# Optimization experiments

Measured on AMD Instinct MI355X. Metric: run time of the kernel, lower is better.

## Reference

```python
import jax, jax.numpy as jnp
import numpy as np

B, EMB, P, K = 8192, 768, 96, 256
D = EMB // P  # dsub = 8


def setup_inputs() -> dict:
    key = jax.random.key(0)
    k1, k2 = jax.random.split(key)
    vecs = jax.random.normal(k1, (B, EMB), dtype=jnp.float32)
    # torch init: uniform(-1, 1)
    codebook = jax.random.uniform(k2, (P, K, D), dtype=jnp.float32, minval=-1.0, maxval=1.0)
    return {"vecs": vecs, "codebook": codebook}


def reference(vecs, codebook):
    b = vecs.shape[0]
    p, k, d = codebook.shape
    v = vecs.reshape(b, p, d)                                  # [B,P,D]
    # squared distances via expanded quadratic (avoids [B,P,K,D] broadcast):
    # ||v-c||^2 = ||v||^2 - 2 v.c + ||c||^2
    dots = jnp.einsum('bpd,pkd->bpk', v, codebook)             # [B,P,K]
    d2 = (jnp.sum(v * v, axis=-1, keepdims=True)               # [B,P,1]
          - 2.0 * dots
          + jnp.sum(codebook * codebook, axis=-1)[None])       # [1,P,K]
    proba = jax.nn.softmax(-d2, axis=-1)                       # [B,P,K]
    # straight-through hard assignment
    idx = jnp.argmax(proba, axis=-1)                           # [B,P]
    hard = jax.nn.one_hot(idx, k, dtype=proba.dtype)           # [B,P,K]
    ste = jax.lax.stop_gradient(hard - proba) + proba
    # reconstruct from codebook
    out = jnp.einsum('bpk,pkd->bpd', ste, codebook).reshape(b, p * d)
    return out
```

## Files before the change

kernel.cpp:

```cpp
#include <hip/hip_runtime.h>


typedef float f32x2 __attribute__((ext_vector_type(2)));
typedef float f32x4 __attribute__((ext_vector_type(4)));

#define TPB 128
#define KBQ 8

namespace {
constexpr int kB   = 8192;
constexpr int kEMB = 768;
constexpr int kP   = 96;
constexpr int kK   = 256;
constexpr int kD   = 8;
constexpr int kNP  = kK / 2;
constexpr int kNCH = kK / 4;
}

__device__ __forceinline__ f32x2 pk_fma(f32x2 a, f32x2 b, f32x2 c) {
    f32x2 d;
    asm("v_pk_fma_f32 %0, %1, %2, %3" : "=v"(d) : "v"(a), "v"(b), "v"(c));
    return d;
}

__device__ __forceinline__ float c2_of(f32x4 lo, f32x4 hi) {
    float t = lo.x * lo.x;
    t = fmaf(lo.y, lo.y, t);
    t = fmaf(lo.z, lo.z, t);
    t = fmaf(lo.w, lo.w, t);
    t = fmaf(hi.x, hi.x, t);
    t = fmaf(hi.y, hi.y, t);
    t = fmaf(hi.z, hi.z, t);
    t = fmaf(hi.w, hi.w, t);
    return t;
}

__global__ __launch_bounds__(TPB, 2)
void pq_argmin_kernel(const float* __restrict__ vecs,
                      const float* __restrict__ codebook,
                      float* __restrict__ out)
{
    __shared__ alignas(16) f32x4 lds_pairs[kNP][4];
    __shared__ alignas(16) f32x2 lds_c2[kNP];

    const int p = blockIdx.y;
    const int t = threadIdx.x;
    const float* __restrict__ cbp = codebook + (size_t)p * kK * kD;
    const f32x4* cb4 = reinterpret_cast<const f32x4*>(cbp);

    {
        f32x4 a0 = cb4[4 * t + 0];
        f32x4 a1 = cb4[4 * t + 1];
        f32x4 b0 = cb4[4 * t + 2];
        f32x4 b1 = cb4[4 * t + 3];
        lds_pairs[t][0] = f32x4{a0.x, b0.x, a0.y, b0.y};
        lds_pairs[t][1] = f32x4{a0.z, b0.z, a0.w, b0.w};
        lds_pairs[t][2] = f32x4{a1.x, b1.x, a1.y, b1.y};
        lds_pairs[t][3] = f32x4{a1.z, b1.z, a1.w, b1.w};
        lds_c2[t] = f32x2{c2_of(a0, a1), c2_of(b0, b1)};
    }

    const int b0q = blockIdx.x * (TPB * KBQ) + t;
    f32x2 vd[KBQ][kD];
#pragma unroll
    for (int q = 0; q < KBQ; ++q) {
        const f32x4* vp = reinterpret_cast<const f32x4*>(
            vecs + (size_t)(b0q + q * TPB) * kEMB + p * kD);
        f32x4 x = vp[0];
        f32x4 y = vp[1];
        float m0 = -2.0f * x.x, m1 = -2.0f * x.y, m2 = -2.0f * x.z,
              m3 = -2.0f * x.w, m4 = -2.0f * y.x, m5 = -2.0f * y.y,
              m6 = -2.0f * y.z, m7 = -2.0f * y.w;
        vd[q][0] = f32x2{m0, m0}; vd[q][1] = f32x2{m1, m1};
        vd[q][2] = f32x2{m2, m2}; vd[q][3] = f32x2{m3, m3};
        vd[q][4] = f32x2{m4, m4}; vd[q][5] = f32x2{m5, m5};
        vd[q][6] = f32x2{m6, m6}; vd[q][7] = f32x2{m7, m7};
    }
    __syncthreads();

    float best[KBQ];
    int   bch[KBQ];
#pragma unroll
    for (int q = 0; q < KBQ; ++q) {
        best[q] = __builtin_inff();
        bch[q] = 0;
    }

#pragma unroll 2
    for (int ch = 0; ch < kNCH; ++ch) {
        f32x4 p0a = lds_pairs[2 * ch][0];
        f32x4 p0b = lds_pairs[2 * ch][1];
        f32x4 p0c = lds_pairs[2 * ch][2];
        f32x4 p0d = lds_pairs[2 * ch][3];
        f32x4 p1a = lds_pairs[2 * ch + 1][0];
        f32x4 p1b = lds_pairs[2 * ch + 1][1];
        f32x4 p1c = lds_pairs[2 * ch + 1][2];
        f32x4 p1d = lds_pairs[2 * ch + 1][3];
        f32x4 cz = *reinterpret_cast<const f32x4*>(&lds_c2[2 * ch]);

#pragma unroll
        for (int q = 0; q < KBQ; ++q) {
            f32x2 a0 = pk_fma(p0a.xy, vd[q][0], cz.xy);
            a0 = pk_fma(p0a.zw, vd[q][1], a0);
            a0 = pk_fma(p0b.xy, vd[q][2], a0);
            a0 = pk_fma(p0b.zw, vd[q][3], a0);
            a0 = pk_fma(p0c.xy, vd[q][4], a0);
            a0 = pk_fma(p0c.zw, vd[q][5], a0);
            a0 = pk_fma(p0d.xy, vd[q][6], a0);
            a0 = pk_fma(p0d.zw, vd[q][7], a0);

            f32x2 a1 = pk_fma(p1a.xy, vd[q][0], cz.zw);
            a1 = pk_fma(p1a.zw, vd[q][1], a1);
            a1 = pk_fma(p1b.xy, vd[q][2], a1);
            a1 = pk_fma(p1b.zw, vd[q][3], a1);
            a1 = pk_fma(p1c.xy, vd[q][4], a1);
            a1 = pk_fma(p1c.zw, vd[q][5], a1);
            a1 = pk_fma(p1d.xy, vd[q][6], a1);
            a1 = pk_fma(p1d.zw, vd[q][7], a1);

            float m = fminf(fminf(fminf(a0.x, a0.y), a1.x), a1.y);
            if (m < best[q]) {
                best[q] = m;
                bch[q] = ch;
            }
        }
    }

#pragma unroll
    for (int q = 0; q < KBQ; ++q) {
        const int base = bch[q] * 4;
        float s[4];
#pragma unroll
        for (int c = 0; c < 4; ++c) {
            f32x4 lo = cb4[2 * (base + c)];
            f32x4 hi = cb4[2 * (base + c) + 1];
            float cc2 = c2_of(lo, hi);
            float s_ = fmaf(lo.x, vd[q][0].x, cc2);
            s_ = fmaf(lo.y, vd[q][1].x, s_);
            s_ = fmaf(lo.z, vd[q][2].x, s_);
            s_ = fmaf(lo.w, vd[q][3].x, s_);
            s_ = fmaf(hi.x, vd[q][4].x, s_);
            s_ = fmaf(hi.y, vd[q][5].x, s_);
            s_ = fmaf(hi.z, vd[q][6].x, s_);
            s_ = fmaf(hi.w, vd[q][7].x, s_);
            s[c] = s_;
        }
        int idx = base;
        bool fnd = (s[0] == best[q]);
#pragma unroll
        for (int c = 1; c < 4; ++c) {
            bool e = (s[c] == best[q]) && !fnd;
            idx = e ? base + c : idx;
            fnd = fnd || (s[c] == best[q]);
        }
        f32x4 r0 = cb4[2 * idx];
        f32x4 r1 = cb4[2 * idx + 1];
        f32x4* op = reinterpret_cast<f32x4*>(
            out + (size_t)(b0q + q * TPB) * kEMB + p * kD);
        op[0] = r0;
        op[1] = r1;
    }
}

extern "C" void kernel_launch(void* const* d_in, const int* in_sizes, int n_in,
                              void* d_out, int out_size, void* d_ws, size_t ws_size,
                              hipStream_t stream)
{
    const float* vecs     = (const float*)d_in[0];
    const float* codebook = (const float*)d_in[1];
    float* out            = (float*)d_out;

    dim3 grid(kB / (TPB * KBQ), kP, 1);
    dim3 block(TPB, 1, 1);
    hipLaunchKernelGGL(pq_argmin_kernel, grid, block, 0, stream,
                       vecs, codebook, out);
}
```

Baseline: 139.0 us.

## Split codebook search across waves and use op_sel packed FMA broadcasts

Each block now has four waves that share the same 512 vectors, and each wave scans a quarter of the 256 codebook entries. Partial minima are merged through LDS after a second barrier, and each wave then finishes two of the eight vector groups. The query registers are halved by using v_pk_fma_f32 op_sel to broadcast the low or high element instead of keeping duplicated pairs, which lowers register pressure and allows a higher occupancy target. The cost is extra LDS traffic, an additional __syncthreads, and redundant vector loads per wave.

```diff
diff --git a/kernel.cpp b/kernel.cpp
--- a/kernel.cpp
+++ b/kernel.cpp
@@ -4,7 +4,7 @@
 typedef float f32x2 __attribute__((ext_vector_type(2)));
 typedef float f32x4 __attribute__((ext_vector_type(4)));
 
-#define TPB 128
+#define TPB 256
 #define KBQ 8
 
 namespace {
@@ -14,12 +14,19 @@
 constexpr int kK   = 256;
 constexpr int kD   = 8;
 constexpr int kNP  = kK / 2;
-constexpr int kNCH = kK / 4;
-}
-
-__device__ __forceinline__ f32x2 pk_fma(f32x2 a, f32x2 b, f32x2 c) {
+constexpr int kChW = 16;
+}
+
+__device__ __forceinline__ f32x2 pk_bl(f32x2 cp, f32x2 qp, f32x2 acc) {
     f32x2 d;
-    asm("v_pk_fma_f32 %0, %1, %2, %3" : "=v"(d) : "v"(a), "v"(b), "v"(c));
+    asm("v_pk_fma_f32 %0, %1, %2, %3 op_sel:[0,0,0] op_sel_hi:[1,0,1]"
+        : "=v"(d) : "v"(cp), "v"(qp), "v"(acc));
+    return d;
+}
+__device__ __forceinline__ f32x2 pk_bh(f32x2 cp, f32x2 qp, f32x2 acc) {
+    f32x2 d;
+    asm("v_pk_fma_f32 %0, %1, %2, %3 op_sel:[0,1,0] op_sel_hi:[1,1,1]"
+        : "=v"(d) : "v"(cp), "v"(qp), "v"(acc));
     return d;
 }
 
@@ -35,20 +42,25 @@
     return t;
 }
 
-__global__ __launch_bounds__(TPB, 2)
+__global__ __launch_bounds__(TPB, 3)
 void pq_argmin_kernel(const float* __restrict__ vecs,
                       const float* __restrict__ codebook,
                       float* __restrict__ out)
 {
     __shared__ alignas(16) f32x4 lds_pairs[kNP][4];
     __shared__ alignas(16) f32x2 lds_c2[kNP];
-
-    const int p = blockIdx.y;
-    const int t = threadIdx.x;
+    __shared__ float lds_best[4][KBQ][64];
+    __shared__ int   lds_gch [4][KBQ][64];
+
+    const int p    = blockIdx.y;
+    const int t    = threadIdx.x;
+    const int lane = t & 63;
+    const int w    = t >> 6;
+
     const float* __restrict__ cbp = codebook + (size_t)p * kK * kD;
     const f32x4* cb4 = reinterpret_cast<const f32x4*>(cbp);
 
-    {
+    if (t < kNP) {
         f32x4 a0 = cb4[4 * t + 0];
         f32x4 a1 = cb4[4 * t + 1];
         f32x4 b0 = cb4[4 * t + 2];
@@ -60,103 +72,120 @@
         lds_c2[t] = f32x2{c2_of(a0, a1), c2_of(b0, b1)};
     }
 
-    const int b0q = blockIdx.x * (TPB * KBQ) + t;
-    f32x2 vd[KBQ][kD];
+    const int b0q = blockIdx.x * (64 * KBQ) + lane;
+    f32x2 qp[KBQ][4];
 #pragma unroll
     for (int q = 0; q < KBQ; ++q) {
         const f32x4* vp = reinterpret_cast<const f32x4*>(
-            vecs + (size_t)(b0q + q * TPB) * kEMB + p * kD);
+            vecs + (size_t)(b0q + q * 64) * kEMB + p * kD);
         f32x4 x = vp[0];
         f32x4 y = vp[1];
-        float m0 = -2.0f * x.x, m1 = -2.0f * x.y, m2 = -2.0f * x.z,
-              m3 = -2.0f * x.w, m4 = -2.0f * y.x, m5 = -2.0f * y.y,
-              m6 = -2.0f * y.z, m7 = -2.0f * y.w;
-        vd[q][0] = f32x2{m0, m0}; vd[q][1] = f32x2{m1, m1};
-        vd[q][2] = f32x2{m2, m2}; vd[q][3] = f32x2{m3, m3};
-        vd[q][4] = f32x2{m4, m4}; vd[q][5] = f32x2{m5, m5};
-        vd[q][6] = f32x2{m6, m6}; vd[q][7] = f32x2{m7, m7};
+        qp[q][0] = f32x2{-2.0f * x.x, -2.0f * x.y};
+        qp[q][1] = f32x2{-2.0f * x.z, -2.0f * x.w};
+        qp[q][2] = f32x2{-2.0f * y.x, -2.0f * y.y};
+        qp[q][3] = f32x2{-2.0f * y.z, -2.0f * y.w};
     }
     __syncthreads();
 
     float best[KBQ];
-    int   bch[KBQ];
+    int   bgch[KBQ];
 #pragma unroll
     for (int q = 0; q < KBQ; ++q) {
         best[q] = __builtin_inff();
-        bch[q] = 0;
+        bgch[q] = w * kChW;
     }
 
 #pragma unroll 2
-    for (int ch = 0; ch < kNCH; ++ch) {
-        f32x4 p0a = lds_pairs[2 * ch][0];
-        f32x4 p0b = lds_pairs[2 * ch][1];
-        f32x4 p0c = lds_pairs[2 * ch][2];
-        f32x4 p0d = lds_pairs[2 * ch][3];
-        f32x4 p1a = lds_pairs[2 * ch + 1][0];
-        f32x4 p1b = lds_pairs[2 * ch + 1][1];
-        f32x4 p1c = lds_pairs[2 * ch + 1][2];
-        f32x4 p1d = lds_pairs[2 * ch + 1][3];
-        f32x4 cz = *reinterpret_cast<const f32x4*>(&lds_c2[2 * ch]);
+    for (int ch = 0; ch < kChW; ++ch) {
+        const int g  = w * kChW + ch;
+        const int pb = 2 * g;
+        f32x4 P0a = lds_pairs[pb][0];
+        f32x4 P0b = lds_pairs[pb][1];
+        f32x4 P0c = lds_pairs[pb][2];
+        f32x4 P0d = lds_pairs[pb][3];
+        f32x4 P1a = lds_pairs[pb + 1][0];
+        f32x4 P1b = lds_pairs[pb + 1][1];
+        f32x4 P1c = lds_pairs[pb + 1][2];
+        f32x4 P1d = lds_pairs[pb + 1][3];
+        f32x4 cz  = *reinterpret_cast<const f32x4*>(&lds_c2[pb]);
 
 #pragma unroll
         for (int q = 0; q < KBQ; ++q) {
-            f32x2 a0 = pk_fma(p0a.xy, vd[q][0], cz.xy);
-            a0 = pk_fma(p0a.zw, vd[q][1], a0);
-            a0 = pk_fma(p0b.xy, vd[q][2], a0);
-            a0 = pk_fma(p0b.zw, vd[q][3], a0);
-            a0 = pk_fma(p0c.xy, vd[q][4], a0);
-            a0 = pk_fma(p0c.zw, vd[q][5], a0);
-            a0 = pk_fma(p0d.xy, vd[q][6], a0);
-            a0 = pk_fma(p0d.zw, vd[q][7], a0);
-
-            f32x2 a1 = pk_fma(p1a.xy, vd[q][0], cz.zw);
-            a1 = pk_fma(p1a.zw, vd[q][1], a1);
-            a1 = pk_fma(p1b.xy, vd[q][2], a1);
-            a1 = pk_fma(p1b.zw, vd[q][3], a1);
-            a1 = pk_fma(p1c.xy, vd[q][4], a1);
-            a1 = pk_fma(p1c.zw, vd[q][5], a1);
-            a1 = pk_fma(p1d.xy, vd[q][6], a1);
-            a1 = pk_fma(p1d.zw, vd[q][7], a1);
+            f32x2 a0 = pk_bl(P0a.xy, qp[q][0], cz.xy);
+            a0 = pk_bh(P0a.zw, qp[q][0], a0);
+            a0 = pk_bl(P0b.xy, qp[q][1], a0);
+            a0 = pk_bh(P0b.zw, qp[q][1], a0);
+            a0 = pk_bl(P0c.xy, qp[q][2], a0);
+            a0 = pk_bh(P0c.zw, qp[q][2], a0);
+            a0 = pk_bl(P0d.xy, qp[q][3], a0);
+            a0 = pk_bh(P0d.zw, qp[q][3], a0);
+
+            f32x2 a1 = pk_bl(P1a.xy, qp[q][0], cz.zw);
+            a1 = pk_bh(P1a.zw, qp[q][0], a1);
+            a1 = pk_bl(P1b.xy, qp[q][1], a1);
+            a1 = pk_bh(P1b.zw, qp[q][1], a1);
+            a1 = pk_bl(P1c.xy, qp[q][2], a1);
+            a1 = pk_bh(P1c.zw, qp[q][2], a1);
+            a1 = pk_bl(P1d.xy, qp[q][3], a1);
+            a1 = pk_bh(P1d.zw, qp[q][3], a1);
 
             float m = fminf(fminf(fminf(a0.x, a0.y), a1.x), a1.y);
             if (m < best[q]) {
                 best[q] = m;
-                bch[q] = ch;
+                bgch[q] = g;
             }
         }
     }
 
 #pragma unroll
     for (int q = 0; q < KBQ; ++q) {
-        const int base = bch[q] * 4;
+        lds_best[w][q][lane] = best[q];
+        lds_gch [w][q][lane] = bgch[q];
+    }
+    __syncthreads();
+
+#pragma unroll
+    for (int qi = 0; qi < 2; ++qi) {
+        const int q = 2 * w + qi;
+        float bb = lds_best[0][q][lane];
+        int   gc = lds_gch [0][q][lane];
+#pragma unroll
+        for (int wv = 1; wv < 4; ++wv) {
+            float b2 = lds_best[wv][q][lane];
+            int   g2 = lds_gch [wv][q][lane];
+            bool c = (b2 < bb);
+            bb = c ? b2 : bb;
+            gc = c ? g2 : gc;
+        }
+        const int base = gc * 4;
         float s[4];
 #pragma unroll
         for (int c = 0; c < 4; ++c) {
             f32x4 lo = cb4[2 * (base + c)];
             f32x4 hi = cb4[2 * (base + c) + 1];
             float cc2 = c2_of(lo, hi);
-            float s_ = fmaf(lo.x, vd[q][0].x, cc2);
-            s_ = fmaf(lo.y, vd[q][1].x, s_);
-            s_ = fmaf(lo.z, vd[q][2].x, s_);
-            s_ = fmaf(lo.w, vd[q][3].x, s_);
-            s_ = fmaf(hi.x, vd[q][4].x, s_);
-            s_ = fmaf(hi.y, vd[q][5].x, s_);
-            s_ = fmaf(hi.z, vd[q][6].x, s_);
-            s_ = fmaf(hi.w, vd[q][7].x, s_);
+            float s_ = fmaf(lo.x, qp[q][0].x, cc2);
+            s_ = fmaf(lo.y, qp[q][0].y, s_);
+            s_ = fmaf(lo.z, qp[q][1].x, s_);
+            s_ = fmaf(lo.w, qp[q][1].y, s_);
+            s_ = fmaf(hi.x, qp[q][2].x, s_);
+            s_ = fmaf(hi.y, qp[q][2].y, s_);
+            s_ = fmaf(hi.z, qp[q][3].x, s_);
+            s_ = fmaf(hi.w, qp[q][3].y, s_);
             s[c] = s_;
         }
         int idx = base;
-        bool fnd = (s[0] == best[q]);
+        bool fnd = (s[0] == bb);
 #pragma unroll
         for (int c = 1; c < 4; ++c) {
-            bool e = (s[c] == best[q]) && !fnd;
+            bool e = (s[c] == bb) && !fnd;
             idx = e ? base + c : idx;
-            fnd = fnd || (s[c] == best[q]);
+            fnd = fnd || (s[c] == bb);
         }
         f32x4 r0 = cb4[2 * idx];
         f32x4 r1 = cb4[2 * idx + 1];
         f32x4* op = reinterpret_cast<f32x4*>(
-            out + (size_t)(b0q + q * TPB) * kEMB + p * kD);
+            out + (size_t)(b0q + q * 64) * kEMB + p * kD);
         op[0] = r0;
         op[1] = r1;
     }
@@ -170,7 +199,7 @@
     const float* codebook = (const float*)d_in[1];
     float* out            = (float*)d_out;
 
-    dim3 grid(kB / (TPB * KBQ), kP, 1);
+    dim3 grid(kB / (64 * KBQ), kP, 1);
     dim3 block(TPB, 1, 1);
     hipLaunchKernelGGL(pq_argmin_kernel, grid, block, 0, stream,
                        vecs, codebook, out);
```

After: 136.5 us. No clear change (-1.9%).
